# Kernel optimization log

Hardware: AMD Instinct MI355X
Metric: run time of the kernel (lower is better)

## Reference

```python
import jax, jax.numpy as jnp
import numpy as np
import math

V, D, H, F, NL, C = 32000, 768, 12, 3072, 6, 10
DK = D // H
EPS = 1e-5


def sinusoidal_pe(L, d_model):
    pos = jnp.arange(L, dtype=jnp.float32)[:, None]
    div = jnp.exp(jnp.arange(0, d_model, 2, dtype=jnp.float32) * (-math.log(10000.0) / d_model))
    pe = jnp.zeros((L, d_model), dtype=jnp.float32)
    pe = pe.at[:, 0::2].set(jnp.sin(pos * div))
    pe = pe.at[:, 1::2].set(jnp.cos(pos * div))
    return pe


def layer_norm(x, g, b):
    mu = jnp.mean(x, axis=-1, keepdims=True)
    var = jnp.mean(jnp.square(x - mu), axis=-1, keepdims=True)
    return (x - mu) / jnp.sqrt(var + EPS) * g + b


def setup_inputs() -> dict:
    key = jax.random.key(0)
    ks = jax.random.split(key, 24)
    s = 0.02
    inp = {
        "input_ids": jax.random.randint(ks[0], (8, 1024), 0, V),
        "mask": jnp.ones((8, 1024), dtype=jnp.int32),
        "emb": jax.random.normal(ks[1], (V, D), dtype=jnp.float32) * s,
        "wq": jax.random.normal(ks[2], (NL, D, D), dtype=jnp.float32) * s,
        "bq": jnp.zeros((NL, D), dtype=jnp.float32),
        "wk": jax.random.normal(ks[3], (NL, D, D), dtype=jnp.float32) * s,
        "bk": jnp.zeros((NL, D), dtype=jnp.float32),
        "wv": jax.random.normal(ks[4], (NL, D, D), dtype=jnp.float32) * s,
        "bv": jnp.zeros((NL, D), dtype=jnp.float32),
        "wo": jax.random.normal(ks[5], (NL, D, D), dtype=jnp.float32) * s,
        "bo": jnp.zeros((NL, D), dtype=jnp.float32),
        "ln1_g": jnp.ones((NL, D), dtype=jnp.float32),
        "ln1_b": jnp.zeros((NL, D), dtype=jnp.float32),
        "w1": jax.random.normal(ks[6], (NL, D, F), dtype=jnp.float32) * s,
        "b1": jnp.zeros((NL, F), dtype=jnp.float32),
        "w2": jax.random.normal(ks[7], (NL, F, D), dtype=jnp.float32) * s,
        "b2": jnp.zeros((NL, D), dtype=jnp.float32),
        "ln2_g": jnp.ones((NL, D), dtype=jnp.float32),
        "ln2_b": jnp.zeros((NL, D), dtype=jnp.float32),
        "cls_w": jax.random.normal(ks[8], (D, C), dtype=jnp.float32) * s,
        "cls_b": jnp.zeros((C,), dtype=jnp.float32),
    }
    return inp


def reference(input_ids, mask, emb, wq, bq, wk, bk, wv, bv, wo, bo,
              ln1_g, ln1_b, w1, b1, w2, b2, ln2_g, ln2_b, cls_w, cls_b):
    B, L = input_ids.shape
    x = emb[input_ids] + sinusoidal_pe(L, D)[None, :, :]  # [B,L,D]
    # mask broadcast: [B,1,1,L] over key positions
    neg = jnp.where(mask[:, None, None, :] == 0, -1e9, 0.0).astype(x.dtype)

    def block(x, p):
        lwq, lbq, lwk, lbk, lwv, lbv, lwo, lbo, g1, bb1, lw1, lb1, lw2, lb2, g2, bb2 = p
        q = (x @ lwq + lbq).reshape(B, L, H, DK)
        k = (x @ lwk + lbk).reshape(B, L, H, DK)
        v = (x @ lwv + lbv).reshape(B, L, H, DK)
        scores = jnp.einsum("blhd,bmhd->bhlm", q, k) / math.sqrt(DK) + neg
        attn = jax.nn.softmax(scores, axis=-1)
        out = jnp.einsum("bhlm,bmhd->blhd", attn, v).reshape(B, L, D)
        out = out @ lwo + lbo
        x = layer_norm(x + out, g1, bb1)
        ff = jnp.maximum(x @ lw1 + lb1, 0.0) @ lw2 + lb2
        x = layer_norm(x + ff, g2, bb2)
        return x, None

    params = (wq, bq, wk, bk, wv, bv, wo, bo, ln1_g, ln1_b, w1, b1, w2, b2, ln2_g, ln2_b)
    x, _ = jax.lax.scan(block, x, params)
    return x[:, 0, :] @ cls_w + cls_b
```

## Files before the change

### kernel.cpp

```cpp
#include <hip/hip_runtime.h>
#include <stdint.h>

typedef unsigned short u16;
typedef __bf16 bf16x8 __attribute__((ext_vector_type(8)));
typedef float f32x4 __attribute__((ext_vector_type(4)));

#define NLAYER 6
#define DM 768
#define NH 12
#define FD 3072
#define NCLS 10
#define BATCH 8
#define SEQ 1024
#define NTOK (BATCH*SEQ)
#define PST 72

__device__ __forceinline__ u16 f2bf(float f) {
  union { float f; unsigned u; } v; v.f = f;
  unsigned u = v.u;
  return (u16)((u + 0x7fffu + ((u >> 16) & 1u)) >> 16);
}

__device__ __forceinline__ void async16(const void* g, void* l) {
  __builtin_amdgcn_global_load_lds(
      (__attribute__((address_space(1))) void*)(void*)g,
      (__attribute__((address_space(3))) void*)l, 16, 0, 0);
}

__global__ __launch_bounds__(256) void transpose_f32_bf16(
    const float* __restrict__ in, u16* __restrict__ out,
    int R, int C, long inLS, long outLS, long outOff)
{
  __shared__ float tile[32][33];
  const float* inp = in + (long)blockIdx.z * inLS;
  u16* outp = out + (long)blockIdx.z * outLS + outOff;
  int c0 = blockIdx.x * 32, r0 = blockIdx.y * 32;
  int tx = threadIdx.x, ty = threadIdx.y;
  #pragma unroll
  for (int j = 0; j < 32; j += 8)
    tile[ty + j][tx] = inp[(long)(r0 + ty + j) * C + c0 + tx];
  __syncthreads();
  #pragma unroll
  for (int j = 0; j < 32; j += 8)
    outp[(long)(c0 + ty + j) * R + r0 + tx] = f2bf(tile[tx][ty + j]);
}

__global__ void concat_bias(const float* __restrict__ bq, const float* __restrict__ bk,
                            const float* __restrict__ bv, float* __restrict__ qkvb)
{
  int i = blockIdx.x * 256 + threadIdx.x;
  if (i >= NLAYER * 2304) return;
  int layer = i / 2304, c = i % 2304;
  float v;
  if (c < 768) v = bq[layer * 768 + c];
  else if (c < 1536) v = bk[layer * 768 + c - 768];
  else v = bv[layer * 768 + c - 1536];
  qkvb[i] = v;
}

__global__ __launch_bounds__(256) void embed_kernel(
    const int* __restrict__ ids, const float* __restrict__ emb,
    float* __restrict__ x, u16* __restrict__ xb)
{
  int e = (blockIdx.x * 256 + threadIdx.x) * 4;
  int d = e % DM;
  int tok = e / DM;
  int l = tok % SEQ;
  int id = ids[tok];
  float4 em = *(const float4*)(emb + (long)id * DM + d);
  const float cexp = -9.210340371976184f / 768.f;
  float div0 = __expf((float)d * cexp);
  float div1 = __expf((float)(d + 2) * cexp);
  float a0 = (float)l * div0, a1 = (float)l * div1;
  em.x += sinf(a0); em.y += cosf(a0);
  em.z += sinf(a1); em.w += cosf(a1);
  *(float4*)(x + e) = em;
  uint2 pk;
  pk.x = f2bf(em.x) | ((unsigned)f2bf(em.y) << 16);
  pk.y = f2bf(em.z) | ((unsigned)f2bf(em.w) << 16);
  *(uint2*)(xb + e) = pk;
}

template<int TM>
__global__ __launch_bounds__(256) void gemm_bt(
    const u16* __restrict__ A, const u16* __restrict__ BT,
    const float* __restrict__ bias,
    float* __restrict__ Cf, u16* __restrict__ Cb, u16* __restrict__ VTout,
    int N, int K, int relu)
{
  constexpr int MI  = TM / 32;
  constexpr int ACH = TM / 8;
  constexpr int NCH = ACH + 16;
  __shared__ __align__(16) u16 As[TM * 64];
  __shared__ __align__(16) u16 Bs[128 * 64];
  int tid = threadIdx.x;
  int wave = tid >> 6, lane = tid & 63;
  int wm = (wave >> 1) * (TM / 2);
  int wn = (wave & 1) * 64;
  int l15 = lane & 15, quad = lane >> 4;
  long mBase = (long)blockIdx.x * TM;
  long nBase = (long)blockIdx.y * 128;
  int r8 = lane >> 3;
  int g8 = ((lane & 7) ^ r8) * 8;

  const u16* gsrc[NCH / 4];
  u16* ldst[NCH / 4];
  #pragma unroll
  for (int idx = 0; idx < NCH / 4; idx++) {
    int c = wave + idx * 4;
    if (c < ACH) {
      gsrc[idx] = A + (mBase + c * 8 + r8) * (long)K + g8;
      ldst[idx] = As + c * 512;
    } else {
      int cc = c - ACH;
      gsrc[idx] = BT + (nBase + cc * 8 + r8) * (long)K + g8;
      ldst[idx] = Bs + cc * 512;
    }
  }
  int sw = l15 & 7;
  int aoff[2], boff[2];
  #pragma unroll
  for (int kc = 0; kc < 2; kc++) {
    aoff[kc] = (wm + l15) * 64 + 8 * ((kc * 4 + quad) ^ sw);
    boff[kc] = (wn + l15) * 64 + 8 * ((kc * 4 + quad) ^ sw);
  }

  f32x4 acc[MI][4] = {};

  for (int k0 = 0; k0 < K; k0 += 64) {
    __syncthreads();
    #pragma unroll
    for (int idx = 0; idx < NCH / 4; idx++)
      async16(gsrc[idx] + k0, ldst[idx]);
    __syncthreads();
    #pragma unroll
    for (int kc = 0; kc < 2; kc++) {
      bf16x8 aF[MI], bF[4];
      #pragma unroll
      for (int i = 0; i < MI; i++) aF[i] = *(const bf16x8*)(As + aoff[kc] + i * 1024);
      #pragma unroll
      for (int j = 0; j < 4; j++)  bF[j] = *(const bf16x8*)(Bs + boff[kc] + j * 1024);
      #pragma unroll
      for (int i = 0; i < MI; i++)
        #pragma unroll
        for (int j = 0; j < 4; j++)
          acc[i][j] = __builtin_amdgcn_mfma_f32_16x16x32_bf16(aF[i], bF[j], acc[i][j], 0, 0, 0);
    }
  }

  #pragma unroll
  for (int j = 0; j < 4; j++) {
    long gn = nBase + wn + j * 16 + l15;
    float bv = bias[gn];
    bool isV = (VTout != nullptr) && (gn >= 1536);
    #pragma unroll
    for (int i = 0; i < MI; i++) {
      long gm0 = mBase + wm + i * 16 + quad * 4;
      if (isV) {
        int h = ((int)gn - 1536) >> 6, dk = (int)gn & 63;
        int bb = (int)(gm0 >> 10), seq = (int)(gm0 & 1023);
        u16* dst = VTout + (((long)(bb * NH + h) * 64 + dk) << 10) + seq;
        uint2 pk;
        pk.x = f2bf(acc[i][j][0] + bv) | ((unsigned)f2bf(acc[i][j][1] + bv) << 16);
        pk.y = f2bf(acc[i][j][2] + bv) | ((unsigned)f2bf(acc[i][j][3] + bv) << 16);
        *(uint2*)dst = pk;
      } else {
        #pragma unroll
        for (int r = 0; r < 4; r++) {
          float v = acc[i][j][r] + bv;
          if (relu) v = fmaxf(v, 0.f);
          long idx = (gm0 + r) * (long)N + gn;
          if (Cf) Cf[idx] = v;
          if (Cb) Cb[idx] = f2bf(v);
        }
      }
    }
  }
}

__global__ __launch_bounds__(256) void attention_mfma(
    const u16* __restrict__ qkvb, const int* __restrict__ mask,
    const u16* __restrict__ vtg, u16* __restrict__ ctxb)
{
  __shared__ __align__(16) u16 Kb[64 * 64];
  __shared__ __align__(16) u16 Vt[64 * 64];
  __shared__ __align__(16) u16 Pl[4][16 * PST];
  __shared__ float negs[64];
  int tid = threadIdx.x;
  int wave = tid >> 6, lane = tid & 63;
  int l15 = lane & 15, quad = lane >> 4;
  int qt = blockIdx.x, bh = blockIdx.y;
  int b = bh / NH, h = bh - b * NH;
  long qtok = (long)b * SEQ + qt * 64;

  bf16x8 aQ[2];
  {
    const u16* qp = qkvb + (qtok + wave * 16 + l15) * 2304 + h * 64 + quad * 8;
    aQ[0] = *(const bf16x8*)qp;
    aQ[1] = *(const bf16x8*)(qp + 32);
  }
  f32x4 oacc[4] = {};
  float lrow[4] = {0.f, 0.f, 0.f, 0.f};

  int r8 = lane >> 3;
  int g8 = ((lane & 7) ^ r8) * 8;
  int ck0 = wave * 2, ck1 = wave * 2 + 1;
  const u16* kg0 = qkvb + ((long)b * SEQ + ck0 * 8 + r8) * 2304 + 768 + h * 64 + g8;
  const u16* kg1 = qkvb + ((long)b * SEQ + ck1 * 8 + r8) * 2304 + 768 + h * 64 + g8;
  const u16* vg0 = vtg + ((long)bh * 64 + ck0 * 8 + r8) * SEQ + g8;
  const u16* vg1 = vtg + ((long)bh * 64 + ck1 * 8 + r8) * SEQ + g8;
  int sw = l15 & 7;
  int soff[2], aoffP[2];
  #pragma unroll
  for (int kc = 0; kc < 2; kc++) {
    soff[kc]  = l15 * 64 + 8 * ((kc * 4 + quad) ^ sw);
    aoffP[kc] = l15 * PST + kc * 32 + quad * 8;
  }
  u16* pw = &Pl[wave][0];

  for (int kt = 0; kt < 16; kt++) {
    __syncthreads();
    async16(kg0 + (long)kt * 64 * 2304, Kb + ck0 * 512);
    async16(kg1 + (long)kt * 64 * 2304, Kb + ck1 * 512);
    async16(vg0 + kt * 64, Vt + ck0 * 512);
    async16(vg1 + kt * 64, Vt + ck1 * 512);
    if (tid < 64) negs[tid] = (mask[(long)b * SEQ + kt * 64 + tid] == 0) ? -1e9f : 0.f;
    __syncthreads();

    f32x4 sa[4] = {};
    #pragma unroll
    for (int kc = 0; kc < 2; kc++)
      #pragma unroll
      for (int n = 0; n < 4; n++) {
        bf16x8 bk = *(const bf16x8*)&Kb[n * 1024 + soff[kc]];
        sa[n] = __builtin_amdgcn_mfma_f32_16x16x32_bf16(aQ[kc], bk, sa[n], 0, 0, 0);
      }
    float ng[4];
    #pragma unroll
    for (int n = 0; n < 4; n++) ng[n] = negs[n * 16 + l15];
    #pragma unroll
    for (int n = 0; n < 4; n++)
      #pragma unroll
      for (int r = 0; r < 4; r++) {
        float s = fminf(sa[n][r] * 0.125f + ng[n], 60.f);
        float p = __expf(s);
        lrow[r] += p;
        pw[(quad * 4 + r) * PST + n * 16 + l15] = f2bf(p);
      }
    #pragma unroll
    for (int kc = 0; kc < 2; kc++) {
      bf16x8 ap = *(const bf16x8*)&pw[aoffP[kc]];
      #pragma unroll
      for (int d = 0; d < 4; d++) {
        bf16x8 bv = *(const bf16x8*)&Vt[d * 1024 + soff[kc]];
        oacc[d] = __builtin_amdgcn_mfma_f32_16x16x32_bf16(ap, bv, oacc[d], 0, 0, 0);
      }
    }
  }

  #pragma unroll
  for (int r = 0; r < 4; r++) {
    lrow[r] += __shfl_xor(lrow[r], 1, 64);
    lrow[r] += __shfl_xor(lrow[r], 2, 64);
    lrow[r] += __shfl_xor(lrow[r], 4, 64);
    lrow[r] += __shfl_xor(lrow[r], 8, 64);
  }
  float inv[4];
  #pragma unroll
  for (int r = 0; r < 4; r++) inv[r] = 1.f / lrow[r];
  #pragma unroll
  for (int d = 0; d < 4; d++)
    #pragma unroll
    for (int r = 0; r < 4; r++)
      pw[(quad * 4 + r) * PST + d * 16 + l15] = f2bf(oacc[d][r] * inv[r]);
  int orow = lane >> 2, ocol = (lane & 3) * 16;
  u16* og = ctxb + (qtok + wave * 16 + orow) * DM + h * 64 + ocol;
  *(uint4*)og       = *(const uint4*)&pw[orow * PST + ocol];
  *(uint4*)(og + 8) = *(const uint4*)&pw[orow * PST + ocol + 8];
}

__global__ __launch_bounds__(64) void ln_residual(
    const float* __restrict__ x, const float* __restrict__ y,
    const float* __restrict__ g, const float* __restrict__ b,
    float* __restrict__ xout, u16* __restrict__ xbout)
{
  long row = blockIdx.x;
  int t = threadIdx.x;
  const float* xr = x + row * DM;
  const float* yr = y + row * DM;
  float v[12];
  float sum = 0.f, sq = 0.f;
  #pragma unroll
  for (int j = 0; j < 3; j++) {
    int d = j * 256 + t * 4;
    float4 a = *(const float4*)(xr + d);
    float4 c = *(const float4*)(yr + d);
    float z0 = a.x + c.x, z1 = a.y + c.y, z2 = a.z + c.z, z3 = a.w + c.w;
    v[j*4+0] = z0; v[j*4+1] = z1; v[j*4+2] = z2; v[j*4+3] = z3;
    sum += z0 + z1 + z2 + z3;
    sq  += z0*z0 + z1*z1 + z2*z2 + z3*z3;
  }
  #pragma unroll
  for (int m = 1; m < 64; m <<= 1) {
    sum += __shfl_xor(sum, m, 64);
    sq  += __shfl_xor(sq,  m, 64);
  }
  float mu = sum * (1.f / 768.f);
  float var = sq * (1.f / 768.f) - mu * mu;
  float rstd = rsqrtf(var + 1e-5f);
  #pragma unroll
  for (int j = 0; j < 3; j++) {
    int d = j * 256 + t * 4;
    float4 gg = *(const float4*)(g + d);
    float4 bb = *(const float4*)(b + d);
    float z0 = (v[j*4+0] - mu) * rstd * gg.x + bb.x;
    float z1 = (v[j*4+1] - mu) * rstd * gg.y + bb.y;
    float z2 = (v[j*4+2] - mu) * rstd * gg.z + bb.z;
    float z3 = (v[j*4+3] - mu) * rstd * gg.w + bb.w;
    float4 fz; fz.x = z0; fz.y = z1; fz.z = z2; fz.w = z3;
    *(float4*)(xout + row * DM + d) = fz;
    uint2 pk;
    pk.x = f2bf(z0) | ((unsigned)f2bf(z1) << 16);
    pk.y = f2bf(z2) | ((unsigned)f2bf(z3) << 16);
    *(uint2*)(xbout + row * DM + d) = pk;
  }
}

__global__ __launch_bounds__(64) void classifier_kernel(
    const float* __restrict__ x, const float* __restrict__ w,
    const float* __restrict__ bias, float* __restrict__ out)
{
  int bc = blockIdx.x;
  int b = bc / NCLS, c = bc % NCLS;
  const float* xr = x + (long)b * SEQ * DM;
  float sum = 0.f;
  for (int d = threadIdx.x; d < DM; d += 64)
    sum += xr[d] * w[d * NCLS + c];
  #pragma unroll
  for (int m = 1; m < 64; m <<= 1) sum += __shfl_xor(sum, m, 64);
  if (threadIdx.x == 0) out[bc] = sum + bias[c];
}

extern "C" void kernel_launch(void* const* d_in, const int* in_sizes, int n_in,
                              void* d_out, int out_size, void* d_ws, size_t ws_size,
                              hipStream_t stream)
{
  const int*   ids  = (const int*)d_in[0];
  const int*   mask = (const int*)d_in[1];
  const float* emb  = (const float*)d_in[2];
  const float* wq   = (const float*)d_in[3];
  const float* bq   = (const float*)d_in[4];
  const float* wk   = (const float*)d_in[5];
  const float* bk   = (const float*)d_in[6];
  const float* wv   = (const float*)d_in[7];
  const float* bv   = (const float*)d_in[8];
  const float* wo   = (const float*)d_in[9];
  const float* bo   = (const float*)d_in[10];
  const float* ln1g = (const float*)d_in[11];
  const float* ln1b = (const float*)d_in[12];
  const float* w1   = (const float*)d_in[13];
  const float* b1   = (const float*)d_in[14];
  const float* w2   = (const float*)d_in[15];
  const float* b2   = (const float*)d_in[16];
  const float* ln2g = (const float*)d_in[17];
  const float* ln2b = (const float*)d_in[18];
  const float* clsw = (const float*)d_in[19];
  const float* clsb = (const float*)d_in[20];

  char* ws = (char*)d_ws;
  size_t off = 0;
  auto alloc = [&](size_t bytes) -> void* {
    void* p = ws + off;
    off += (bytes + 255) & ~(size_t)255;
    return p;
  };
  float* X     = (float*)alloc((size_t)NTOK * DM * 4);
  u16*   XB    = (u16*)  alloc((size_t)NTOK * DM * 2);
  u16*   QKVB16= (u16*)  alloc((size_t)NTOK * 2304 * 2);
  u16*   VT    = (u16*)  alloc((size_t)96 * 64 * SEQ * 2);
  u16*   CTXB  = (u16*)  alloc((size_t)NTOK * DM * 2);
  u16*   H1B   = (u16*)  alloc((size_t)NTOK * FD * 2);
  float* SCR   = (float*)alloc((size_t)NTOK * DM * 4);
  u16*   WQKVT = (u16*)  alloc((size_t)NLAYER * 2304 * 768 * 2);
  u16*   WOT   = (u16*)  alloc((size_t)NLAYER * 768 * 768 * 2);
  u16*   W1T   = (u16*)  alloc((size_t)NLAYER * 3072 * 768 * 2);
  u16*   W2T   = (u16*)  alloc((size_t)NLAYER * 768 * 3072 * 2);
  float* QKVB  = (float*)alloc((size_t)NLAYER * 2304 * 4);

  dim3 tb(32, 8);
  transpose_f32_bf16<<<dim3(24, 24, 6), tb, 0, stream>>>(wq, WQKVT, 768, 768, 768L*768, 2304L*768, 0);
  transpose_f32_bf16<<<dim3(24, 24, 6), tb, 0, stream>>>(wk, WQKVT, 768, 768, 768L*768, 2304L*768, 768L*768);
  transpose_f32_bf16<<<dim3(24, 24, 6), tb, 0, stream>>>(wv, WQKVT, 768, 768, 768L*768, 2304L*768, 1536L*768);
  transpose_f32_bf16<<<dim3(24, 24, 6), tb, 0, stream>>>(wo, WOT, 768, 768, 768L*768, 768L*768, 0);
  transpose_f32_bf16<<<dim3(96, 24, 6), tb, 0, stream>>>(w1, W1T, 768, 3072, 768L*3072, 3072L*768, 0);
  transpose_f32_bf16<<<dim3(24, 96, 6), tb, 0, stream>>>(w2, W2T, 3072, 768, 3072L*768, 768L*3072, 0);
  concat_bias<<<(NLAYER * 2304 + 255) / 256, 256, 0, stream>>>(bq, bk, bv, QKVB);
  embed_kernel<<<NTOK * DM / 1024, 256, 0, stream>>>(ids, emb, X, XB);

  for (int L = 0; L < NLAYER; L++) {
    gemm_bt<128><<<dim3(64, 18), 256, 0, stream>>>(
        XB, WQKVT + (size_t)L * 2304 * 768, QKVB + L * 2304,
        nullptr, QKVB16, VT, 2304, 768, 0);
    attention_mfma<<<dim3(16, 96), 256, 0, stream>>>(QKVB16, mask, VT, CTXB);
    gemm_bt<64><<<dim3(128, 6), 256, 0, stream>>>(
        CTXB, WOT + (size_t)L * 768 * 768, bo + L * 768,
        SCR, nullptr, nullptr, 768, 768, 0);
    ln_residual<<<NTOK, 64, 0, stream>>>(X, SCR, ln1g + L * 768, ln1b + L * 768, X, XB);
    gemm_bt<128><<<dim3(64, 24), 256, 0, stream>>>(
        XB, W1T + (size_t)L * 3072 * 768, b1 + L * 3072,
        nullptr, H1B, nullptr, 3072, 768, 1);
    gemm_bt<64><<<dim3(128, 6), 256, 0, stream>>>(
        H1B, W2T + (size_t)L * 768 * 3072, b2 + L * 768,
        SCR, nullptr, nullptr, 768, 3072, 0);
    ln_residual<<<NTOK, 64, 0, stream>>>(X, SCR, ln2g + L * 768, ln2b + L * 768, X, XB);
  }
  classifier_kernel<<<80, 64, 0, stream>>>(X, clsw, clsb, (float*)d_out);
}
```

Before: 2.022 ms.

## Pre-pack weights into MFMA fragment layout and stream B directly to registers

Replaces the weight transposes with a pack kernel that stores each 16x32 bf16 B-fragment contiguously in the order the MFMA lanes consume it. The GEMM then loads B straight from global memory into registers, prefetched one K-step ahead, and no longer stages B through LDS, which cuts LDS traffic and footprint. It also adds an LDS-staged epilogue for bf16 outputs so that rows are written with 16-byte coalesced stores. In exchange it adds register pressure and relies on the register prefetch to hide global latency for B.

```diff
diff --git a/kernel.cpp b/kernel.cpp
--- a/kernel.cpp
+++ b/kernel.cpp
@@ -27,22 +27,28 @@
       (__attribute__((address_space(3))) void*)l, 16, 0, 0);
 }
 
-__global__ __launch_bounds__(256) void transpose_f32_bf16(
-    const float* __restrict__ in, u16* __restrict__ out,
-    int R, int C, long inLS, long outLS, long outOff)
-{
-  __shared__ float tile[32][33];
-  const float* inp = in + (long)blockIdx.z * inLS;
-  u16* outp = out + (long)blockIdx.z * outLS + outOff;
-  int c0 = blockIdx.x * 32, r0 = blockIdx.y * 32;
-  int tx = threadIdx.x, ty = threadIdx.y;
-  #pragma unroll
-  for (int j = 0; j < 32; j += 8)
-    tile[ty + j][tx] = inp[(long)(r0 + ty + j) * C + c0 + tx];
-  __syncthreads();
-  #pragma unroll
-  for (int j = 0; j < 32; j += 8)
-    outp[(long)(c0 + ty + j) * R + r0 + tx] = f2bf(tile[tx][ty + j]);
+__global__ __launch_bounds__(256) void pack_weights(
+    const float* __restrict__ src, u16* __restrict__ dst,
+    int K, int N, long srcLS, long dstLS, int ntOff, int ntCount)
+{
+  int z = blockIdx.z;
+  int K32 = K >> 5;
+  int fid = blockIdx.x * 4 + (threadIdx.x >> 6);
+  int ntL = fid / K32, kc = fid - ntL * K32;
+  if (ntL >= ntCount) return;
+  int lane = threadIdx.x & 63;
+  int l15 = lane & 15, quad = lane >> 4;
+  int n = ntL * 16 + l15;
+  const float* s = src + (long)z * srcLS + (long)(kc * 32 + quad * 8) * N + n;
+  unsigned pk[4];
+  #pragma unroll
+  for (int j = 0; j < 4; j++) {
+    u16 a = f2bf(s[(2 * j) * (long)N]);
+    u16 b = f2bf(s[(2 * j + 1) * (long)N]);
+    pk[j] = (unsigned)a | ((unsigned)b << 16);
+  }
+  u16* d = dst + (long)z * dstLS + ((long)(ntOff + ntL) * K32 + kc) * 512 + lane * 8;
+  *(uint4*)d = *(uint4*)pk;
 }
 
 __global__ void concat_bias(const float* __restrict__ bq, const float* __restrict__ bk,
@@ -82,17 +88,16 @@
 }
 
 template<int TM>
-__global__ __launch_bounds__(256) void gemm_bt(
-    const u16* __restrict__ A, const u16* __restrict__ BT,
+__global__ __launch_bounds__(256) void gemm_pk(
+    const u16* __restrict__ A, const u16* __restrict__ WP,
     const float* __restrict__ bias,
     float* __restrict__ Cf, u16* __restrict__ Cb, u16* __restrict__ VTout,
     int N, int K, int relu)
 {
   constexpr int MI  = TM / 32;
   constexpr int ACH = TM / 8;
-  constexpr int NCH = ACH + 16;
-  __shared__ __align__(16) u16 As[TM * 64];
-  __shared__ __align__(16) u16 Bs[128 * 64];
+  constexpr int ASZ = (TM == 128) ? 9216 : TM * 64;
+  __shared__ __align__(16) u16 As[ASZ];
   int tid = threadIdx.x;
   int wave = tid >> 6, lane = tid & 63;
   int wm = (wave >> 1) * (TM / 2);
@@ -100,78 +105,134 @@
   int l15 = lane & 15, quad = lane >> 4;
   long mBase = (long)blockIdx.x * TM;
   long nBase = (long)blockIdx.y * 128;
+  int K32 = K >> 5;
   int r8 = lane >> 3;
   int g8 = ((lane & 7) ^ r8) * 8;
 
-  const u16* gsrc[NCH / 4];
-  u16* ldst[NCH / 4];
-  #pragma unroll
-  for (int idx = 0; idx < NCH / 4; idx++) {
+  const u16* gsrc[ACH / 4];
+  u16* ldst[ACH / 4];
+  #pragma unroll
+  for (int idx = 0; idx < ACH / 4; idx++) {
     int c = wave + idx * 4;
-    if (c < ACH) {
-      gsrc[idx] = A + (mBase + c * 8 + r8) * (long)K + g8;
-      ldst[idx] = As + c * 512;
-    } else {
-      int cc = c - ACH;
-      gsrc[idx] = BT + (nBase + cc * 8 + r8) * (long)K + g8;
-      ldst[idx] = Bs + cc * 512;
-    }
+    gsrc[idx] = A + (mBase + c * 8 + r8) * (long)K + g8;
+    ldst[idx] = As + c * 512;
   }
   int sw = l15 & 7;
-  int aoff[2], boff[2];
-  #pragma unroll
-  for (int kc = 0; kc < 2; kc++) {
+  int aoff[2];
+  #pragma unroll
+  for (int kc = 0; kc < 2; kc++)
     aoff[kc] = (wm + l15) * 64 + 8 * ((kc * 4 + quad) ^ sw);
-    boff[kc] = (wn + l15) * 64 + 8 * ((kc * 4 + quad) ^ sw);
-  }
+
+  const u16* bpp = WP + ((long)(nBase >> 4) + (wn >> 4)) * K32 * 512 + lane * 8;
+  uint4 bnx[2][4];
+  #pragma unroll
+  for (int kc = 0; kc < 2; kc++)
+    #pragma unroll
+    for (int j = 0; j < 4; j++)
+      bnx[kc][j] = *(const uint4*)(bpp + ((long)j * K32 + kc) * 512);
 
   f32x4 acc[MI][4] = {};
 
   for (int k0 = 0; k0 < K; k0 += 64) {
     __syncthreads();
     #pragma unroll
-    for (int idx = 0; idx < NCH / 4; idx++)
+    for (int idx = 0; idx < ACH / 4; idx++)
       async16(gsrc[idx] + k0, ldst[idx]);
     __syncthreads();
+
+    uint4 bcur[2][4];
+    #pragma unroll
+    for (int kc = 0; kc < 2; kc++)
+      #pragma unroll
+      for (int j = 0; j < 4; j++)
+        bcur[kc][j] = bnx[kc][j];
+    if (k0 + 64 < K) {
+      int nch = (k0 >> 5) + 2;
+      #pragma unroll
+      for (int kc = 0; kc < 2; kc++)
+        #pragma unroll
+        for (int j = 0; j < 4; j++)
+          bnx[kc][j] = *(const uint4*)(bpp + ((long)j * K32 + nch + kc) * 512);
+    }
     #pragma unroll
     for (int kc = 0; kc < 2; kc++) {
-      bf16x8 aF[MI], bF[4];
+      bf16x8 aF[MI];
       #pragma unroll
       for (int i = 0; i < MI; i++) aF[i] = *(const bf16x8*)(As + aoff[kc] + i * 1024);
-      #pragma unroll
-      for (int j = 0; j < 4; j++)  bF[j] = *(const bf16x8*)(Bs + boff[kc] + j * 1024);
       #pragma unroll
       for (int i = 0; i < MI; i++)
         #pragma unroll
-        for (int j = 0; j < 4; j++)
-          acc[i][j] = __builtin_amdgcn_mfma_f32_16x16x32_bf16(aF[i], bF[j], acc[i][j], 0, 0, 0);
-    }
-  }
-
-  #pragma unroll
-  for (int j = 0; j < 4; j++) {
-    long gn = nBase + wn + j * 16 + l15;
-    float bv = bias[gn];
-    bool isV = (VTout != nullptr) && (gn >= 1536);
-    #pragma unroll
-    for (int i = 0; i < MI; i++) {
-      long gm0 = mBase + wm + i * 16 + quad * 4;
-      if (isV) {
-        int h = ((int)gn - 1536) >> 6, dk = (int)gn & 63;
+        for (int j = 0; j < 4; j++) {
+          bf16x8 bb = *(bf16x8*)&bcur[kc][j];
+          acc[i][j] = __builtin_amdgcn_mfma_f32_16x16x32_bf16(aF[i], bb, acc[i][j], 0, 0, 0);
+        }
+    }
+  }
+
+  if (VTout != nullptr && nBase >= 1536) {
+    #pragma unroll
+    for (int j = 0; j < 4; j++) {
+      long gn = nBase + wn + j * 16 + l15;
+      float bv = bias[gn];
+      int h = ((int)gn - 1536) >> 6, dk = (int)gn & 63;
+      #pragma unroll
+      for (int i = 0; i < MI; i++) {
+        long gm0 = mBase + wm + i * 16 + quad * 4;
         int bb = (int)(gm0 >> 10), seq = (int)(gm0 & 1023);
         u16* dst = VTout + (((long)(bb * NH + h) * 64 + dk) << 10) + seq;
         uint2 pk;
         pk.x = f2bf(acc[i][j][0] + bv) | ((unsigned)f2bf(acc[i][j][1] + bv) << 16);
         pk.y = f2bf(acc[i][j][2] + bv) | ((unsigned)f2bf(acc[i][j][3] + bv) << 16);
         *(uint2*)dst = pk;
-      } else {
+      }
+    }
+  } else if (Cb != nullptr) {
+    if constexpr (TM == 128) {
+      __syncthreads();
+      u16* ep = As + wave * 2304;
+      float bvj[4];
+      #pragma unroll
+      for (int j = 0; j < 4; j++) bvj[j] = bias[nBase + wn + j * 16 + l15];
+      #pragma unroll
+      for (int h = 0; h < 2; h++) {
+        #pragma unroll
+        for (int ii = 0; ii < 2; ii++) {
+          int i = 2 * h + ii;
+          #pragma unroll
+          for (int j = 0; j < 4; j++)
+            #pragma unroll
+            for (int r = 0; r < 4; r++) {
+              float v = acc[i][j][r] + bvj[j];
+              if (relu) v = fmaxf(v, 0.f);
+              ep[(ii * 16 + quad * 4 + r) * 72 + j * 16 + l15] = f2bf(v);
+            }
+        }
+        #pragma unroll
+        for (int rr = 0; rr < 2; rr++) {
+          int row = (lane >> 2) + rr * 16;
+          int c = (lane & 3) * 16;
+          uint4 d0 = *(const uint4*)&ep[row * 72 + c];
+          uint4 d1 = *(const uint4*)&ep[row * 72 + c + 8];
+          long gm = mBase + wm + h * 32 + row;
+          u16* dst = Cb + gm * (long)N + nBase + wn + c;
+          *(uint4*)dst = d0;
+          *(uint4*)(dst + 8) = d1;
+        }
+      }
+    }
+  } else {
+    #pragma unroll
+    for (int j = 0; j < 4; j++) {
+      long gn = nBase + wn + j * 16 + l15;
+      float bv = bias[gn];
+      #pragma unroll
+      for (int i = 0; i < MI; i++) {
+        long gm0 = mBase + wm + i * 16 + quad * 4;
         #pragma unroll
         for (int r = 0; r < 4; r++) {
           float v = acc[i][j][r] + bv;
           if (relu) v = fmaxf(v, 0.f);
-          long idx = (gm0 + r) * (long)N + gn;
-          if (Cf) Cf[idx] = v;
-          if (Cb) Cb[idx] = f2bf(v);
+          Cf[(gm0 + r) * (long)N + gn] = v;
         }
       }
     }
@@ -374,43 +435,43 @@
     off += (bytes + 255) & ~(size_t)255;
     return p;
   };
-  float* X     = (float*)alloc((size_t)NTOK * DM * 4);
-  u16*   XB    = (u16*)  alloc((size_t)NTOK * DM * 2);
-  u16*   QKVB16= (u16*)  alloc((size_t)NTOK * 2304 * 2);
-  u16*   VT    = (u16*)  alloc((size_t)96 * 64 * SEQ * 2);
-  u16*   CTXB  = (u16*)  alloc((size_t)NTOK * DM * 2);
-  u16*   H1B   = (u16*)  alloc((size_t)NTOK * FD * 2);
-  float* SCR   = (float*)alloc((size_t)NTOK * DM * 4);
-  u16*   WQKVT = (u16*)  alloc((size_t)NLAYER * 2304 * 768 * 2);
-  u16*   WOT   = (u16*)  alloc((size_t)NLAYER * 768 * 768 * 2);
-  u16*   W1T   = (u16*)  alloc((size_t)NLAYER * 3072 * 768 * 2);
-  u16*   W2T   = (u16*)  alloc((size_t)NLAYER * 768 * 3072 * 2);
-  float* QKVB  = (float*)alloc((size_t)NLAYER * 2304 * 4);
-
-  dim3 tb(32, 8);
-  transpose_f32_bf16<<<dim3(24, 24, 6), tb, 0, stream>>>(wq, WQKVT, 768, 768, 768L*768, 2304L*768, 0);
-  transpose_f32_bf16<<<dim3(24, 24, 6), tb, 0, stream>>>(wk, WQKVT, 768, 768, 768L*768, 2304L*768, 768L*768);
-  transpose_f32_bf16<<<dim3(24, 24, 6), tb, 0, stream>>>(wv, WQKVT, 768, 768, 768L*768, 2304L*768, 1536L*768);
-  transpose_f32_bf16<<<dim3(24, 24, 6), tb, 0, stream>>>(wo, WOT, 768, 768, 768L*768, 768L*768, 0);
-  transpose_f32_bf16<<<dim3(96, 24, 6), tb, 0, stream>>>(w1, W1T, 768, 3072, 768L*3072, 3072L*768, 0);
-  transpose_f32_bf16<<<dim3(24, 96, 6), tb, 0, stream>>>(w2, W2T, 3072, 768, 3072L*768, 768L*3072, 0);
+  float* X      = (float*)alloc((size_t)NTOK * DM * 4);
+  u16*   XB     = (u16*)  alloc((size_t)NTOK * DM * 2);
+  u16*   QKVB16 = (u16*)  alloc((size_t)NTOK * 2304 * 2);
+  u16*   VT     = (u16*)  alloc((size_t)96 * 64 * SEQ * 2);
+  u16*   CTXB   = (u16*)  alloc((size_t)NTOK * DM * 2);
+  u16*   H1B    = (u16*)  alloc((size_t)NTOK * FD * 2);
+  float* SCR    = (float*)alloc((size_t)NTOK * DM * 4);
+  u16*   WQKV_P = (u16*)  alloc((size_t)NLAYER * 144 * 24 * 512 * 2);
+  u16*   WO_P   = (u16*)  alloc((size_t)NLAYER * 48 * 24 * 512 * 2);
+  u16*   W1_P   = (u16*)  alloc((size_t)NLAYER * 192 * 24 * 512 * 2);
+  u16*   W2_P   = (u16*)  alloc((size_t)NLAYER * 48 * 96 * 512 * 2);
+  float* QKVB   = (float*)alloc((size_t)NLAYER * 2304 * 4);
+
+  const long LSW = 768L * 768;
+  pack_weights<<<dim3(288, 1, 6), 256, 0, stream>>>(wq, WQKV_P, 768, 768, LSW, 144L*24*512, 0, 48);
+  pack_weights<<<dim3(288, 1, 6), 256, 0, stream>>>(wk, WQKV_P, 768, 768, LSW, 144L*24*512, 48, 48);
+  pack_weights<<<dim3(288, 1, 6), 256, 0, stream>>>(wv, WQKV_P, 768, 768, LSW, 144L*24*512, 96, 48);
+  pack_weights<<<dim3(288, 1, 6), 256, 0, stream>>>(wo, WO_P, 768, 768, LSW, 48L*24*512, 0, 48);
+  pack_weights<<<dim3(1152, 1, 6), 256, 0, stream>>>(w1, W1_P, 768, 3072, 768L*3072, 192L*24*512, 0, 192);
+  pack_weights<<<dim3(1152, 1, 6), 256, 0, stream>>>(w2, W2_P, 3072, 768, 3072L*768, 48L*96*512, 0, 48);
   concat_bias<<<(NLAYER * 2304 + 255) / 256, 256, 0, stream>>>(bq, bk, bv, QKVB);
   embed_kernel<<<NTOK * DM / 1024, 256, 0, stream>>>(ids, emb, X, XB);
 
   for (int L = 0; L < NLAYER; L++) {
-    gemm_bt<128><<<dim3(64, 18), 256, 0, stream>>>(
-        XB, WQKVT + (size_t)L * 2304 * 768, QKVB + L * 2304,
+    gemm_pk<128><<<dim3(64, 18), 256, 0, stream>>>(
+        XB, WQKV_P + (size_t)L * 144 * 24 * 512, QKVB + L * 2304,
         nullptr, QKVB16, VT, 2304, 768, 0);
     attention_mfma<<<dim3(16, 96), 256, 0, stream>>>(QKVB16, mask, VT, CTXB);
-    gemm_bt<64><<<dim3(128, 6), 256, 0, stream>>>(
-        CTXB, WOT + (size_t)L * 768 * 768, bo + L * 768,
+    gemm_pk<64><<<dim3(128, 6), 256, 0, stream>>>(
+        CTXB, WO_P + (size_t)L * 48 * 24 * 512, bo + L * 768,
         SCR, nullptr, nullptr, 768, 768, 0);
     ln_residual<<<NTOK, 64, 0, stream>>>(X, SCR, ln1g + L * 768, ln1b + L * 768, X, XB);
-    gemm_bt<128><<<dim3(64, 24), 256, 0, stream>>>(
-        XB, W1T + (size_t)L * 3072 * 768, b1 + L * 3072,
+    gemm_pk<128><<<dim3(64, 24), 256, 0, stream>>>(
+        XB, W1_P + (size_t)L * 192 * 24 * 512, b1 + L * 3072,
         nullptr, H1B, nullptr, 3072, 768, 1);
-    gemm_bt<64><<<dim3(128, 6), 256, 0, stream>>>(
-        H1B, W2T + (size_t)L * 768 * 3072, b2 + L * 768,
+    gemm_pk<64><<<dim3(128, 6), 256, 0, stream>>>(
+        H1B, W2_P + (size_t)L * 48 * 96 * 512, b2 + L * 768,
         SCR, nullptr, nullptr, 768, 3072, 0);
     ln_residual<<<NTOK, 64, 0, stream>>>(X, SCR, ln2g + L * 768, ln2b + L * 768, X, XB);
   }
```

Result: slower. 2.093 ms (+3.6%).
